# Kernel optimization log

Measured on AMD Instinct MI355X. Metric: run time of the kernel, lower is better.

The kernel has to match this reference:

```python
import jax, jax.numpy as jnp
import numpy as np

B, T, DIM = 4, 2048, 1024
H, DH = 16, 64  # num_heads, dim_head; weight_dim = H*DH = 1024
SCALE = DIM ** (-0.5)  # note: original scales by dim**-0.5, not dim_head**-0.5


def setup_inputs() -> dict:
    key = jax.random.key(0)
    k1, k2, k3 = jax.random.split(key, 3)
    x = jax.random.normal(k1, (B, T, DIM), dtype=jnp.float32)
    w_qkv = jax.random.normal(k2, (3 * H * DH, DIM), dtype=jnp.float32) * (DIM ** -0.5)
    w_out = jax.random.normal(k3, (DIM, H * DH), dtype=jnp.float32) * ((H * DH) ** -0.5)
    b_out = jnp.zeros((DIM,), dtype=jnp.float32)
    return {"x": x, "w_qkv": w_qkv, "w_out": w_out, "b_out": b_out}


def reference(x, w_qkv, w_out, b_out):
    # qkv: [b, t, 3*H*DH] (torch Linear: x @ W^T)
    qkv = jnp.einsum('btc,oc->bto', x, w_qkv)
    # rearrange 'b t (d k h) -> k b h t d' with k=3, h=H: d is the OUTERMOST
    # factor of the flattened axis, then k, then h (h fastest-varying).
    qkv = qkv.reshape(B, T, DH, 3, H)          # [b, t, d, k, h]
    qkv = jnp.transpose(qkv, (3, 0, 4, 1, 2))   # [k, b, h, t, d]
    q, k, v = qkv[0], qkv[1], qkv[2]
    # scores: [b, h, t, t]
    attn = jnp.einsum('bhid,bhjd->bhij', q, k) * SCALE
    attn = jax.nn.softmax(attn, axis=-1)
    out = jnp.einsum('bhij,bhjd->bhid', attn, v)           # [b, h, t, d]
    out = jnp.transpose(out, (0, 2, 1, 3)).reshape(B, T, H * DH)  # 'b h t d -> b t (h d)'
    return jnp.einsum('btc,oc->bto', out, w_out) + b_out
```

## Files before the change

### kernel.cpp

```cpp
#include <hip/hip_runtime.h>
#include <hip/hip_bf16.h>


typedef __attribute__((ext_vector_type(8))) short short8;
typedef __attribute__((ext_vector_type(4))) float floatx4;
typedef __attribute__((ext_vector_type(16))) float floatx16;

static __device__ __forceinline__ floatx4 mfma16(short8 a, short8 b, floatx4 c) {
    return __builtin_amdgcn_mfma_f32_16x16x32_bf16(a, b, c, 0, 0, 0);
}
static __device__ __forceinline__ floatx16 mfma32(short8 a, short8 b, floatx16 c) {
    return __builtin_amdgcn_mfma_f32_32x32x16_bf16(a, b, c, 0, 0, 0);
}

static __device__ __forceinline__ unsigned short f2bf_bits(float f) {
    __hip_bfloat16 h = __float2bfloat16(f);
    return *reinterpret_cast<unsigned short*>(&h);
}

static __device__ __forceinline__ float fast_exp2(float x) {
#if __has_builtin(__builtin_amdgcn_exp2f)
    return __builtin_amdgcn_exp2f(x);
#else
    return exp2f(x);
#endif
}

static __device__ __forceinline__ unsigned cvt_pk_bf16(float lo, float hi) {
    unsigned r;
    asm("v_cvt_pk_bf16_f32 %0, %1, %2" : "=v"(r) : "v"(lo), "v"(hi));
    return r;
}

static __device__ __forceinline__ void plane32_swap(unsigned& x, unsigned& y) {
#if __has_builtin(__builtin_amdgcn_permlane32_swap)
    typedef unsigned int uintx2 __attribute__((ext_vector_type(2)));
    uintx2 r = __builtin_amdgcn_permlane32_swap(x, y, false, false);
    x = r[0];
    y = r[1];
#else
    asm volatile("v_permlane32_swap_b32 %0, %1" : "+v"(x), "+v"(y));
#endif
}

#define GLD16(gptr, ldsptr)                                                  \
    __builtin_amdgcn_global_load_lds(                                        \
        (const __attribute__((address_space(1))) void*)(gptr),               \
        (__attribute__((address_space(3))) void*)(ldsptr), 16, 0, 0)

__global__ __launch_bounds__(256) void k_cvt(
    const float* __restrict__ src, unsigned short* __restrict__ dst, int n4)
{
    typedef __attribute__((ext_vector_type(4))) unsigned short ushort4v;
    for (int i = blockIdx.x * blockDim.x + threadIdx.x; i < n4;
         i += gridDim.x * blockDim.x) {
        const float4 v = ((const float4*)src)[i];
        ushort4v o;
        o.x = f2bf_bits(v.x);
        o.y = f2bf_bits(v.y);
        o.z = f2bf_bits(v.z);
        o.w = f2bf_bits(v.w);
        ((ushort4v*)dst)[i] = o;
    }
}

__global__ __launch_bounds__(256) void k_qkv(
    const unsigned short* __restrict__ x,
    const unsigned short* __restrict__ wq,
    unsigned short* __restrict__ qb,
    unsigned short* __restrict__ kb,
    unsigned short* __restrict__ vb)
{
    __shared__ unsigned short SM[16384];

    const int tid  = threadIdx.x;
    const int wave = tid >> 6, lane = tid & 63;
    const int quad = lane >> 4, l16 = lane & 15;
    const int wm = wave >> 1, wn = wave & 1;

    const int fid  = blockIdx.y * 24 + blockIdx.x;
    const int nfid = (fid & 7) * 192 + (fid >> 3);
    const int bx = nfid % 24;
    const int m0 = (nfid / 24) * 128;
    const int kk = bx >> 3;
    const int cb = bx & 7;

    const int srow = lane >> 2;
    const int sc8  = (lane & 3) * 8;
    const int row0 = wave * 32 + srow;
    const int row1 = row0 + 16;
    int bn0, bn1;
    if (kk < 2) {
        bn0 = (row0 & 63) * 48 + kk * 16 + cb * 2 + (row0 >> 6);
        bn1 = (row1 & 63) * 48 + kk * 16 + cb * 2 + (row1 >> 6);
    } else {
        bn0 = (cb * 8 + (row0 >> 4)) * 48 + 32 + (row0 & 15);
        bn1 = (cb * 8 + (row1 >> 4)) * 48 + 32 + (row1 & 15);
    }

    floatx4 acc[4][4];
#pragma unroll
    for (int i = 0; i < 4; i++)
#pragma unroll
        for (int j = 0; j < 4; j++) acc[i][j] = (floatx4){0.f, 0.f, 0.f, 0.f};

#define QKV_STAGE(BUF, K0)                                                        \
    do {                                                                          \
        GLD16(&x[(m0 + row0) * 1024 + (K0) + sc8],                                \
              &SM[(BUF) * 8192 + (wave * 32) * 32]);                              \
        GLD16(&x[(m0 + row1) * 1024 + (K0) + sc8],                                \
              &SM[(BUF) * 8192 + (wave * 32 + 16) * 32]);                         \
        GLD16(&wq[bn0 * 1024 + (K0) + sc8],                                       \
              &SM[(BUF) * 8192 + 4096 + (wave * 32) * 32]);                       \
        GLD16(&wq[bn1 * 1024 + (K0) + sc8],                                       \
              &SM[(BUF) * 8192 + 4096 + (wave * 32 + 16) * 32]);                  \
    } while (0)

    QKV_STAGE(0, 0);
    int buf = 0;
    for (int k0 = 0; k0 < 1024; k0 += 32) {
        __syncthreads();
        if (k0 + 32 < 1024) QKV_STAGE(buf ^ 1, k0 + 32);

        const unsigned short* Ab = &SM[buf * 8192];
        const unsigned short* Bb = &SM[buf * 8192 + 4096];
        short8 af[4], bfv[4];
#pragma unroll
        for (int mi = 0; mi < 4; mi++)
            af[mi] = *(const short8*)&Ab[(wm * 64 + mi * 16 + l16) * 32 + quad * 8];
#pragma unroll
        for (int ni = 0; ni < 4; ni++)
            bfv[ni] = *(const short8*)&Bb[(wn * 64 + ni * 16 + l16) * 32 + quad * 8];
#pragma unroll
        for (int mi = 0; mi < 4; mi++)
#pragma unroll
            for (int ni = 0; ni < 4; ni++)
                acc[mi][ni] = mfma16(af[mi], bfv[ni], acc[mi][ni]);
        buf ^= 1;
    }
    __syncthreads();

    if (kk == 2) {
#pragma unroll
        for (int ni = 0; ni < 4; ni++) {
            const int d = cb * 8 + wn * 4 + ni;
#pragma unroll
            for (int mi = 0; mi < 4; mi++) {
                const int m  = m0 + wm * 64 + mi * 16 + quad * 4;
                const int b  = m >> 11;
                const int tt = m & 2047;
                ushort4 pk;
                pk.x = f2bf_bits(acc[mi][ni][0]);
                pk.y = f2bf_bits(acc[mi][ni][1]);
                pk.z = f2bf_bits(acc[mi][ni][2]);
                pk.w = f2bf_bits(acc[mi][ni][3]);
                *(ushort4*)&vb[((b * 16 + l16) * 64 + d) * 2048 + tt] = pk;
            }
        }
    } else {
        const float scale = (kk == 0) ? 0.045084220027780106f : 1.0f;
        unsigned short* dst = (kk == 0) ? qb : kb;
        const int b = m0 >> 11, tt0 = m0 & 2047;
#pragma unroll
        for (int s = 0; s < 2; s++) {
            if (wn == s) {
#pragma unroll
                for (int ni = 0; ni < 4; ni++) {
                    const int d = ni * 16 + l16;
#pragma unroll
                    for (int mi = 0; mi < 4; mi++) {
                        const int tl = wm * 64 + mi * 16 + quad * 4;
#pragma unroll
                        for (int r = 0; r < 4; r++)
                            SM[(tl + r) * 72 + d] = f2bf_bits(acc[mi][ni][r] * scale);
                    }
                }
            }
            __syncthreads();
#pragma unroll
            for (int u = 0; u < 4; u++) {
                const int w  = tid + u * 256;
                const int tl = w >> 3;
                const int ch = (w & 7) * 8;
                *(uint4*)&dst[((b * 16 + cb * 2 + s) * 2048 + tt0 + tl) * 64 + ch] =
                    *(const uint4*)&SM[tl * 72 + ch];
            }
            __syncthreads();
        }
    }
#undef QKV_STAGE
}

__global__ __launch_bounds__(256, 2) void k_attn(
    const unsigned short* __restrict__ qt,
    const unsigned short* __restrict__ kt,
    const unsigned short* __restrict__ vg,
    __hip_bfloat16* __restrict__ og)
{
    __shared__ unsigned short Ks[64 * 72];
    __shared__ unsigned short Vt[64 * 72];

    const int tid  = threadIdx.x;
    const int wave = tid >> 6, lane = tid & 63;
    const int l31  = lane & 31, hi = lane >> 5;
    const int blk = blockIdx.x;
    const int bh  = (blk & 7) | ((blk >> 6) << 3);
    const int q0  = ((blk >> 3) & 7) * 256;
    const int qr  = q0 + wave * 64;

    short8 qf[2][4];
#pragma unroll
    for (int qb2 = 0; qb2 < 2; qb2++)
#pragma unroll
        for (int ks = 0; ks < 4; ks++)
            qf[qb2][ks] = *(const short8*)
                &qt[(bh * 2048 + qr + qb2 * 32 + l31) * 64 + ks * 16 + hi * 8];

    float lsum[2] = {0.f, 0.f};
    floatx16 o[2][2];
#pragma unroll
    for (int qb2 = 0; qb2 < 2; qb2++)
#pragma unroll
        for (int db = 0; db < 2; db++)
#pragma unroll
            for (int r = 0; r < 16; r++) o[qb2][db][r] = 0.f;

    const int sr = tid >> 2, sc = (tid & 3) * 16;

    uint4 rka = *(const uint4*)&kt[(bh * 2048 + sr) * 64 + sc];
    uint4 rkb = *(const uint4*)&kt[(bh * 2048 + sr) * 64 + sc + 8];
    uint4 rva = *(const uint4*)&vg[(bh * 64 + sr) * 2048 + sc];
    uint4 rvb = *(const uint4*)&vg[(bh * 64 + sr) * 2048 + sc + 8];

    for (int j0 = 0; j0 < 2048; j0 += 64) {
        *(uint4*)&Ks[sr * 72 + sc]     = rka;
        *(uint4*)&Ks[sr * 72 + sc + 8] = rkb;
        *(uint4*)&Vt[sr * 72 + sc]     = rva;
        *(uint4*)&Vt[sr * 72 + sc + 8] = rvb;
        __syncthreads();
        if (j0 + 64 < 2048) {
            rka = *(const uint4*)&kt[(bh * 2048 + j0 + 64 + sr) * 64 + sc];
            rkb = *(const uint4*)&kt[(bh * 2048 + j0 + 64 + sr) * 64 + sc + 8];
            rva = *(const uint4*)&vg[(bh * 64 + sr) * 2048 + j0 + 64 + sc];
            rvb = *(const uint4*)&vg[(bh * 64 + sr) * 2048 + j0 + 64 + sc + 8];
        }

#pragma unroll
        for (int kb2 = 0; kb2 < 2; kb2++) {
            short8 kf[4];
#pragma unroll
            for (int ks = 0; ks < 4; ks++)
                kf[ks] = *(const short8*)
                    &Ks[(kb2 * 32 + l31) * 72 + ks * 16 + hi * 8];

            floatx16 st[2];
#pragma unroll
            for (int qb2 = 0; qb2 < 2; qb2++)
#pragma unroll
                for (int r = 0; r < 16; r++) st[qb2][r] = 0.f;
            __builtin_amdgcn_s_setprio(1);
#pragma unroll
            for (int ks = 0; ks < 4; ks++)
#pragma unroll
                for (int qb2 = 0; qb2 < 2; qb2++)
                    st[qb2] = mfma32(kf[ks], qf[qb2][ks], st[qb2]);
            __builtin_amdgcn_s_setprio(0);

            short8 paf[2][2];
#pragma unroll
            for (int qb2 = 0; qb2 < 2; qb2++) {
                float p[16];
#pragma unroll
                for (int r = 0; r < 16; r++) p[r] = fast_exp2(st[qb2][r]);
                lsum[qb2] += ((p[0] + p[1]) + (p[2] + p[3])) +
                             ((p[4] + p[5]) + (p[6] + p[7])) +
                             ((p[8] + p[9]) + (p[10] + p[11])) +
                             ((p[12] + p[13]) + (p[14] + p[15]));
#pragma unroll
                for (int hf = 0; hf < 2; hf++) {
                    const int r0 = hf * 8;
                    unsigned c01 = cvt_pk_bf16(p[r0 + 0], p[r0 + 1]);
                    unsigned c23 = cvt_pk_bf16(p[r0 + 2], p[r0 + 3]);
                    unsigned c45 = cvt_pk_bf16(p[r0 + 4], p[r0 + 5]);
                    unsigned c67 = cvt_pk_bf16(p[r0 + 6], p[r0 + 7]);
                    plane32_swap(c01, c45);
                    plane32_swap(c23, c67);
                    uint4 t4 = {c01, c23, c45, c67};
                    paf[qb2][hf] = *reinterpret_cast<short8*>(&t4);
                }
            }

            short8 vf[2][2];
#pragma unroll
            for (int db = 0; db < 2; db++)
#pragma unroll
                for (int hf = 0; hf < 2; hf++)
                    vf[db][hf] = *(const short8*)
                        &Vt[(db * 32 + l31) * 72 + kb2 * 32 + hf * 16 + hi * 8];
            __builtin_amdgcn_s_setprio(1);
#pragma unroll
            for (int qb2 = 0; qb2 < 2; qb2++)
#pragma unroll
                for (int db = 0; db < 2; db++)
#pragma unroll
                    for (int hf = 0; hf < 2; hf++)
                        o[qb2][db] = mfma32(paf[qb2][hf], vf[db][hf], o[qb2][db]);
            __builtin_amdgcn_s_setprio(0);
        }
        __syncthreads();
    }

    lsum[0] += __shfl_xor(lsum[0], 32);
    lsum[1] += __shfl_xor(lsum[1], 32);

    const int b = bh >> 4, h = bh & 15;
#pragma unroll
    for (int qb2 = 0; qb2 < 2; qb2++) {
#pragma unroll
        for (int r = 0; r < 16; r++) {
            const int qrl = (r & 3) + 8 * (r >> 2) + 4 * hi;
            const float inv = 1.0f / __shfl(lsum[qb2], qrl);
            const int t = qr + qb2 * 32 + qrl;
#pragma unroll
            for (int db = 0; db < 2; db++)
                og[(b * 2048 + t) * 1024 + h * 64 + db * 32 + l31] =
                    __float2bfloat16(o[qb2][db][r] * inv);
        }
    }
}

__global__ __launch_bounds__(256) void k_out(
    const unsigned short* __restrict__ a,
    const unsigned short* __restrict__ wq,
    const float* __restrict__ bias,
    float* __restrict__ out)
{
    __shared__ unsigned short SM[16384];

    const int tid  = threadIdx.x;
    const int wave = tid >> 6, lane = tid & 63;
    const int quad = lane >> 4, l16 = lane & 15;
    const int wm = wave >> 1, wn = wave & 1;

    const int fid  = blockIdx.y * 8 + blockIdx.x;
    const int nfid = (fid & 7) * 64 + (fid >> 3);
    const int n0 = (nfid & 7) * 128;
    const int m0 = (nfid >> 3) * 128;

    const int srow = lane >> 2;
    const int sc8  = (lane & 3) * 8;
    const int row0 = wave * 32 + srow;
    const int row1 = row0 + 16;

    floatx4 acc[4][4];
#pragma unroll
    for (int i = 0; i < 4; i++)
#pragma unroll
        for (int j = 0; j < 4; j++) acc[i][j] = (floatx4){0.f, 0.f, 0.f, 0.f};

#define OUT_STAGE(BUF, K0)                                                        \
    do {                                                                          \
        GLD16(&a[(m0 + row0) * 1024 + (K0) + sc8],                                \
              &SM[(BUF) * 8192 + (wave * 32) * 32]);                              \
        GLD16(&a[(m0 + row1) * 1024 + (K0) + sc8],                                \
              &SM[(BUF) * 8192 + (wave * 32 + 16) * 32]);                         \
        GLD16(&wq[(n0 + row0) * 1024 + (K0) + sc8],                               \
              &SM[(BUF) * 8192 + 4096 + (wave * 32) * 32]);                       \
        GLD16(&wq[(n0 + row1) * 1024 + (K0) + sc8],                               \
              &SM[(BUF) * 8192 + 4096 + (wave * 32 + 16) * 32]);                  \
    } while (0)

    OUT_STAGE(0, 0);
    int buf = 0;
    for (int k0 = 0; k0 < 1024; k0 += 32) {
        __syncthreads();
        if (k0 + 32 < 1024) OUT_STAGE(buf ^ 1, k0 + 32);

        const unsigned short* Ab = &SM[buf * 8192];
        const unsigned short* Bb = &SM[buf * 8192 + 4096];
        short8 af[4], bfv[4];
#pragma unroll
        for (int mi = 0; mi < 4; mi++)
            af[mi] = *(const short8*)&Ab[(wm * 64 + mi * 16 + l16) * 32 + quad * 8];
#pragma unroll
        for (int ni = 0; ni < 4; ni++)
            bfv[ni] = *(const short8*)&Bb[(wn * 64 + ni * 16 + l16) * 32 + quad * 8];
#pragma unroll
        for (int mi = 0; mi < 4; mi++)
#pragma unroll
            for (int ni = 0; ni < 4; ni++)
                acc[mi][ni] = mfma16(af[mi], bfv[ni], acc[mi][ni]);
        buf ^= 1;
    }
#undef OUT_STAGE

#pragma unroll
    for (int ni = 0; ni < 4; ni++) {
        const int col = n0 + wn * 64 + ni * 16 + l16;
        const float bv = bias[col];
#pragma unroll
        for (int mi = 0; mi < 4; mi++) {
            const int mbase = m0 + wm * 64 + mi * 16 + quad * 4;
#pragma unroll
            for (int r = 0; r < 4; r++)
                out[(mbase + r) * 1024 + col] = acc[mi][ni][r] + bv;
        }
    }
}

extern "C" void kernel_launch(void* const* d_in, const int* in_sizes, int n_in,
                              void* d_out, int out_size, void* d_ws, size_t ws_size,
                              hipStream_t stream) {
    const float* x    = (const float*)d_in[0];
    const float* wqkv = (const float*)d_in[1];
    const float* wout = (const float*)d_in[2];
    const float* bout = (const float*)d_in[3];
    float* out = (float*)d_out;

    unsigned short* ws = (unsigned short*)d_ws;
    unsigned short* xb    = ws;
    unsigned short* wqkvb = xb + 8388608;
    unsigned short* woutb = wqkvb + 3145728;
    unsigned short* qb    = woutb + 1048576;
    unsigned short* kb    = qb + 8388608;
    unsigned short* vb    = kb + 8388608;
    unsigned short* ob    = vb + 8388608;

    k_cvt<<<2048, 256, 0, stream>>>(x,    xb,    8388608 / 4);
    k_cvt<<<1024, 256, 0, stream>>>(wqkv, wqkvb, 3145728 / 4);
    k_cvt<<<512,  256, 0, stream>>>(wout, woutb, 1048576 / 4);

    k_qkv<<<dim3(24, 64), 256, 0, stream>>>(xb, wqkvb, qb, kb, vb);
    k_attn<<<512, 256, 0, stream>>>(qb, kb, vb, (__hip_bfloat16*)ob);
    k_out<<<dim3(8, 64), 256, 0, stream>>>(ob, woutb, bout, out);
}
```

Before: 254.2 us.

## Double-buffer K/V LDS tiles in attention and merge conversion launches

The attention kernel now keeps two LDS buffers for the K and V tiles. The next tile is written into the alternate buffer while the current one is consumed, so each iteration needs one barrier instead of two. The three fp32-to-bf16 conversion launches are merged into a single kernel that branches on the index to pick its source array. The price is double the attention LDS footprint, which could limit occupancy, plus manual waitcnt and sched_barrier handling that the compiler can no longer schedule around.

```diff
diff --git a/kernel.cpp b/kernel.cpp
--- a/kernel.cpp
+++ b/kernel.cpp
@@ -48,19 +48,28 @@
         (const __attribute__((address_space(1))) void*)(gptr),               \
         (__attribute__((address_space(3))) void*)(ldsptr), 16, 0, 0)
 
-__global__ __launch_bounds__(256) void k_cvt(
-    const float* __restrict__ src, unsigned short* __restrict__ dst, int n4)
+__global__ __launch_bounds__(256) void k_cvt3(
+    const float* __restrict__ s0,
+    const float* __restrict__ s1,
+    const float* __restrict__ s2,
+    unsigned short* __restrict__ dst)
 {
     typedef __attribute__((ext_vector_type(4))) unsigned short ushort4v;
-    for (int i = blockIdx.x * blockDim.x + threadIdx.x; i < n4;
+    for (int i = blockIdx.x * blockDim.x + threadIdx.x; i < 3145728;
          i += gridDim.x * blockDim.x) {
-        const float4 v = ((const float4*)src)[i];
+        const float4* sp;
+        unsigned short* dp;
+        int li;
+        if (i < 2097152)      { sp = (const float4*)s0; dp = dst;            li = i; }
+        else if (i < 2883584) { sp = (const float4*)s1; dp = dst + 8388608;  li = i - 2097152; }
+        else                  { sp = (const float4*)s2; dp = dst + 11534336; li = i - 2883584; }
+        const float4 v = sp[li];
         ushort4v o;
         o.x = f2bf_bits(v.x);
         o.y = f2bf_bits(v.y);
         o.z = f2bf_bits(v.z);
         o.w = f2bf_bits(v.w);
-        ((ushort4v*)dst)[i] = o;
+        ((ushort4v*)dp)[li] = o;
     }
 }
 
@@ -123,7 +132,7 @@
         if (k0 + 32 < 1024) QKV_STAGE(buf ^ 1, k0 + 32);
 
         const unsigned short* Ab = &SM[buf * 8192];
-        const unsigned short* Bb = &SM[buf * 8192 + 4096];
+        const unsigned short* Bb = Ab + 4096;
         short8 af[4], bfv[4];
 #pragma unroll
         for (int mi = 0; mi < 4; mi++)
@@ -197,8 +206,8 @@
     const unsigned short* __restrict__ vg,
     __hip_bfloat16* __restrict__ og)
 {
-    __shared__ unsigned short Ks[64 * 72];
-    __shared__ unsigned short Vt[64 * 72];
+    __shared__ unsigned short Ks[2 * 64 * 72];
+    __shared__ unsigned short Vt[2 * 64 * 72];
 
     const int tid  = threadIdx.x;
     const int wave = tid >> 6, lane = tid & 63;
@@ -231,19 +240,36 @@
     uint4 rkb = *(const uint4*)&kt[(bh * 2048 + sr) * 64 + sc + 8];
     uint4 rva = *(const uint4*)&vg[(bh * 64 + sr) * 2048 + sc];
     uint4 rvb = *(const uint4*)&vg[(bh * 64 + sr) * 2048 + sc + 8];
-
+    *(uint4*)&Ks[sr * 72 + sc]     = rka;
+    *(uint4*)&Ks[sr * 72 + sc + 8] = rkb;
+    *(uint4*)&Vt[sr * 72 + sc]     = rva;
+    *(uint4*)&Vt[sr * 72 + sc + 8] = rvb;
+    rka = *(const uint4*)&kt[(bh * 2048 + 64 + sr) * 64 + sc];
+    rkb = *(const uint4*)&kt[(bh * 2048 + 64 + sr) * 64 + sc + 8];
+    rva = *(const uint4*)&vg[(bh * 64 + sr) * 2048 + 64 + sc];
+    rvb = *(const uint4*)&vg[(bh * 64 + sr) * 2048 + 64 + sc + 8];
+    asm volatile("s_waitcnt lgkmcnt(0)" ::: "memory");
+    __builtin_amdgcn_sched_barrier(0);
+
+    int c = 0;
     for (int j0 = 0; j0 < 2048; j0 += 64) {
-        *(uint4*)&Ks[sr * 72 + sc]     = rka;
-        *(uint4*)&Ks[sr * 72 + sc + 8] = rkb;
-        *(uint4*)&Vt[sr * 72 + sc]     = rva;
-        *(uint4*)&Vt[sr * 72 + sc + 8] = rvb;
-        __syncthreads();
+        __builtin_amdgcn_s_barrier();
+        __builtin_amdgcn_sched_barrier(0);
+        const int nx = c ^ 1;
         if (j0 + 64 < 2048) {
-            rka = *(const uint4*)&kt[(bh * 2048 + j0 + 64 + sr) * 64 + sc];
-            rkb = *(const uint4*)&kt[(bh * 2048 + j0 + 64 + sr) * 64 + sc + 8];
-            rva = *(const uint4*)&vg[(bh * 64 + sr) * 2048 + j0 + 64 + sc];
-            rvb = *(const uint4*)&vg[(bh * 64 + sr) * 2048 + j0 + 64 + sc + 8];
-        }
+            *(uint4*)&Ks[nx * 4608 + sr * 72 + sc]     = rka;
+            *(uint4*)&Ks[nx * 4608 + sr * 72 + sc + 8] = rkb;
+            *(uint4*)&Vt[nx * 4608 + sr * 72 + sc]     = rva;
+            *(uint4*)&Vt[nx * 4608 + sr * 72 + sc + 8] = rvb;
+        }
+        if (j0 + 128 < 2048) {
+            rka = *(const uint4*)&kt[(bh * 2048 + j0 + 128 + sr) * 64 + sc];
+            rkb = *(const uint4*)&kt[(bh * 2048 + j0 + 128 + sr) * 64 + sc + 8];
+            rva = *(const uint4*)&vg[(bh * 64 + sr) * 2048 + j0 + 128 + sc];
+            rvb = *(const uint4*)&vg[(bh * 64 + sr) * 2048 + j0 + 128 + sc + 8];
+        }
+        const unsigned short* Kc = &Ks[c * 4608];
+        const unsigned short* Vc = &Vt[c * 4608];
 
 #pragma unroll
         for (int kb2 = 0; kb2 < 2; kb2++) {
@@ -251,7 +277,7 @@
 #pragma unroll
             for (int ks = 0; ks < 4; ks++)
                 kf[ks] = *(const short8*)
-                    &Ks[(kb2 * 32 + l31) * 72 + ks * 16 + hi * 8];
+                    &Kc[(kb2 * 32 + l31) * 72 + ks * 16 + hi * 8];
 
             floatx16 st[2];
 #pragma unroll
@@ -272,10 +298,10 @@
                 float p[16];
 #pragma unroll
                 for (int r = 0; r < 16; r++) p[r] = fast_exp2(st[qb2][r]);
-                lsum[qb2] += ((p[0] + p[1]) + (p[2] + p[3])) +
-                             ((p[4] + p[5]) + (p[6] + p[7])) +
-                             ((p[8] + p[9]) + (p[10] + p[11])) +
-                             ((p[12] + p[13]) + (p[14] + p[15]));
+                lsum[qb2] += (((p[0] + p[1]) + (p[2] + p[3])) +
+                              ((p[4] + p[5]) + (p[6] + p[7]))) +
+                             (((p[8] + p[9]) + (p[10] + p[11])) +
+                              ((p[12] + p[13]) + (p[14] + p[15])));
 #pragma unroll
                 for (int hf = 0; hf < 2; hf++) {
                     const int r0 = hf * 8;
@@ -296,7 +322,7 @@
 #pragma unroll
                 for (int hf = 0; hf < 2; hf++)
                     vf[db][hf] = *(const short8*)
-                        &Vt[(db * 32 + l31) * 72 + kb2 * 32 + hf * 16 + hi * 8];
+                        &Vc[(db * 32 + l31) * 72 + kb2 * 32 + hf * 16 + hi * 8];
             __builtin_amdgcn_s_setprio(1);
 #pragma unroll
             for (int qb2 = 0; qb2 < 2; qb2++)
@@ -307,7 +333,9 @@
                         o[qb2][db] = mfma32(paf[qb2][hf], vf[db][hf], o[qb2][db]);
             __builtin_amdgcn_s_setprio(0);
         }
-        __syncthreads();
+        asm volatile("s_waitcnt lgkmcnt(0)" ::: "memory");
+        __builtin_amdgcn_sched_barrier(0);
+        c ^= 1;
     }
 
     lsum[0] += __shfl_xor(lsum[0], 32);
@@ -377,7 +405,7 @@
         if (k0 + 32 < 1024) OUT_STAGE(buf ^ 1, k0 + 32);
 
         const unsigned short* Ab = &SM[buf * 8192];
-        const unsigned short* Bb = &SM[buf * 8192 + 4096];
+        const unsigned short* Bb = Ab + 4096;
         short8 af[4], bfv[4];
 #pragma unroll
         for (int mi = 0; mi < 4; mi++)
@@ -426,9 +454,7 @@
     unsigned short* vb    = kb + 8388608;
     unsigned short* ob    = vb + 8388608;
 
-    k_cvt<<<2048, 256, 0, stream>>>(x,    xb,    8388608 / 4);
-    k_cvt<<<1024, 256, 0, stream>>>(wqkv, wqkvb, 3145728 / 4);
-    k_cvt<<<512,  256, 0, stream>>>(wout, woutb, 1048576 / 4);
+    k_cvt3<<<2048, 256, 0, stream>>>(x, wqkv, wout, ws);
 
     k_qkv<<<dim3(24, 64), 256, 0, stream>>>(xb, wqkvb, qb, kb, vb);
     k_attn<<<512, 256, 0, stream>>>(qb, kb, vb, (__hip_bfloat16*)ob);
```

Result: no change. 258.0 us (+1.5%).
